# Optimization experiments

Hardware: AMD Instinct MI355X
Metric: run time of the kernel (lower is better)

Reference implementation:

```python
import jax, jax.numpy as jnp
import numpy as np

B, N, NPOINT, NSAMPLE = 8, 8192, 2048, 32
RADIUS = 0.4
C_IN = 64
MLP = [64, 64, 128]
EPS = 1e-5
BIG = 1e10


def setup_inputs() -> dict:
    key = jax.random.key(0)
    ks = jax.random.split(key, 2 + 4 * len(MLP))
    inp = {
        'xyz': jax.random.normal(ks[0], (B, N, 3), jnp.float32),
        'features': jax.random.normal(ks[1], (B, C_IN, N), jnp.float32),
    }
    last_c = C_IN + 3
    j = 2
    for i, out_c in enumerate(MLP):
        inp[f'w{i}'] = jax.random.normal(ks[j], (out_c, last_c), jnp.float32) * (1.0 / np.sqrt(last_c)); j += 1
        inp[f'b{i}'] = jax.random.normal(ks[j], (out_c,), jnp.float32) * 0.01; j += 1
        inp[f'g{i}'] = 1.0 + 0.01 * jax.random.normal(ks[j], (out_c,), jnp.float32); j += 1
        inp[f'bt{i}'] = 0.01 * jax.random.normal(ks[j], (out_c,), jnp.float32); j += 1
        last_c = out_c
    return inp


def fps(xyz, m):
    # Farthest point sampling; deterministic start at index 0 (torch uses randint).
    b, n, _ = xyz.shape

    def step(carry, _):
        dist, far = carry
        centroid = jnp.take_along_axis(xyz, far[:, None, None], axis=1)  # [B,1,3]
        d = jnp.sum((xyz - centroid) ** 2, axis=-1)                      # [B,N]
        dist = jnp.minimum(dist, d)
        new_far = jnp.argmax(dist, axis=1)
        return (dist, new_far), far

    init = (jnp.full((b, n), BIG, xyz.dtype), jnp.zeros((b,), jnp.int32))
    _, idxs = jax.lax.scan(step, init, None, length=m)
    return jnp.transpose(idxs)  # [B,m]


def ball_query(xyz, centroids, radius, k):
    # Euclidean cdist via the (a-b)^2 = a^2 + b^2 - 2ab expansion.
    x2 = jnp.sum(xyz * xyz, axis=-1)            # [B,N]
    c2 = jnp.sum(centroids * centroids, axis=-1)  # [B,M]
    d2 = c2[:, :, None] + x2[:, None, :] - 2.0 * jnp.einsum('bmd,bnd->bmn', centroids, xyz)
    d = jnp.sqrt(jnp.maximum(d2, 0.0))           # [B,M,N]
    dm = jnp.where(d <= radius, d, BIG)
    _, idx = jax.lax.top_k(-dm, k)               # k smallest distances
    return idx                                   # [B,M,K]


def gather_points(x, idx):
    # x: [B,N,C], idx: [B,M,K] -> [B,M,K,C]
    b = x.shape[0]
    return x[jnp.arange(b)[:, None, None], idx]


def reference(xyz, features, w0, b0, g0, bt0, w1, b1, g1, bt1, w2, b2, g2, bt2):
    idx = fps(xyz, NPOINT)                                   # [B,M]
    new_xyz = jnp.take_along_axis(xyz, idx[:, :, None], axis=1)  # [B,M,3]
    knn_idx = ball_query(xyz, new_xyz, RADIUS, NSAMPLE)      # [B,M,K]
    grouped_xyz = gather_points(xyz, knn_idx)                # [B,M,K,3]
    grouped_xyz_norm = grouped_xyz - new_xyz[:, :, None, :]
    grouped_feat = gather_points(jnp.transpose(features, (0, 2, 1)), knn_idx)  # [B,M,K,C]
    feat = jnp.concatenate([grouped_xyz_norm, grouped_feat], axis=-1)          # [B,M,K,C+3]

    for w, b, g, bt in ((w0, b0, g0, bt0), (w1, b1, g1, bt1), (w2, b2, g2, bt2)):
        feat = jnp.einsum('bmkc,oc->bmko', feat, w) + b      # 1x1 conv
        mu = jnp.mean(feat, axis=(0, 1, 2))                  # BN, training-mode batch stats
        var = jnp.mean((feat - mu) ** 2, axis=(0, 1, 2))
        feat = (feat - mu) * jax.lax.rsqrt(var + EPS) * g + bt
        feat = jax.nn.relu(feat)

    new_feat = jnp.max(feat, axis=2)                         # max over neighbors -> [B,M,C_out]
    return new_xyz, jnp.transpose(new_feat, (0, 2, 1))       # [B,M,3], [B,C_out,M]
```

## Files before the change

kernel.cpp:

```cpp
#include <hip/hip_runtime.h>
#include <hip/hip_bf16.h>
#include <stdint.h>

typedef unsigned short u16;
typedef unsigned int   u32;
typedef unsigned long long u64;
typedef float v2f __attribute__((ext_vector_type(2)));
typedef __attribute__((ext_vector_type(8))) short bf16x8;
typedef __attribute__((ext_vector_type(4))) float f32x4;

#define B_    8
#define N_    8192
#define M_    2048
#define NS_   32
#define CIN_  64
#define ROWS_ (B_*M_*NS_)
#define BIGF  1e10f
#define EPSF  1e-5f
#define INV_ROWS (1.0f/524288.0f)

__device__ __forceinline__ u16 f2bf(float f){
  u32 x=__float_as_uint(f);
  return (u16)((x + 0x7FFFu + ((x>>16)&1u))>>16);
}
__device__ __forceinline__ float bf2f(u16 u){ return __uint_as_float(((u32)u)<<16); }

__device__ __forceinline__ u64 wave_max_key(u64 k){
#define DPP_LVL(CTRL) { \
    u32 lo_=(u32)__builtin_amdgcn_update_dpp(0,(int)(u32)k,(CTRL),0xF,0xF,true); \
    u32 hi_=(u32)__builtin_amdgcn_update_dpp(0,(int)(u32)(k>>32),(CTRL),0xF,0xF,true); \
    u64 o_=((u64)hi_<<32)|(u64)lo_; \
    k=(o_>k)?o_:k; }
  DPP_LVL(0x111)
  DPP_LVL(0x112)
  DPP_LVL(0x114)
  DPP_LVL(0x118)
  DPP_LVL(0x142)
  DPP_LVL(0x143)
#undef DPP_LVL
  return k;
}

__global__ __launch_bounds__(256) void k_prep(
    const float* w0,const float* b0,const float* g0,const float* bt0,
    const float* w1,const float* b1,const float* g1,const float* bt1,
    const float* w2,const float* b2,const float* g2,const float* bt2,
    float* biasf,float* gf,float* btf,float* stats,
    u16* Wb0h, u16* Wb0l, u16* Wb1h, u16* Wb1l, u16* Wb2h, u16* Wb2l)
{
  int tid=threadIdx.x;
  for (int i=tid;i<768;i+=256) stats[i]=0.f;
  for (int i=tid;i<6144;i+=256){
    int e=i&7, lane=(i>>3)&63, idx=i>>9;
    int tn=idx/3, k0=idx%3;
    int col = tn*16 + (lane&15);
    int k   = k0*32 + ((lane>>4)&3)*8 + e;
    float v = 0.f;
    if (k < 64)            v = w0[col*67 + 3 + k];
    else if (k < 67)       v = w0[col*67 + (k-64)];
    u16 hib = f2bf(v);
    Wb0h[i] = hib;
    Wb0l[i] = f2bf(v - bf2f(hib));
  }
  for (int i=tid;i<4096;i+=256){
    int e=i&7, lane=(i>>3)&63, k0=(i>>9)&1, tn=i>>10;
    int col = tn*16 + (lane&15);
    int k   = k0*32 + ((lane>>4)&3)*8 + e;
    float v = w1[col*64 + k];
    u16 hib = f2bf(v);
    Wb1h[i] = hib;
    Wb1l[i] = f2bf(v - bf2f(hib));
  }
  for (int i=tid;i<8192;i+=256){
    int e=i&7, lane=(i>>3)&63, k0=(i>>9)&1, tn=i>>10;
    int col = tn*16 + (lane&15);
    int k   = k0*32 + ((lane>>4)&3)*8 + e;
    float v = w2[col*64 + k];
    u16 hib = f2bf(v);
    Wb2h[i] = hib;
    Wb2l[i] = f2bf(v - bf2f(hib));
  }
  if (tid<64){
    biasf[0*128+tid]=b0[tid]; gf[0*128+tid]=g0[tid]; btf[0*128+tid]=bt0[tid];
    biasf[1*128+tid]=b1[tid]; gf[1*128+tid]=g1[tid]; btf[1*128+tid]=bt1[tid];
  }
  if (tid<128){
    biasf[2*128+tid]=b2[tid]; gf[2*128+tid]=g2[tid]; btf[2*128+tid]=bt2[tid];
  }
}

__global__ __launch_bounds__(256) void k_tr(const float* __restrict__ feats, u16* __restrict__ featT)
{
  __shared__ float t[64][65];
  int bb=blockIdx.y, n0=blockIdx.x*64, tid=threadIdx.x;
  int a=tid&63, q=tid>>6;
  const float* fp = feats + (size_t)bb*CIN_*N_;
  #pragma unroll
  for (int s=0;s<16;s++){ int c=q*16+s; t[c][a]=fp[(size_t)c*N_ + n0 + a]; }
  __syncthreads();
  u16* op = featT + (size_t)bb*N_*CIN_;
  #pragma unroll
  for (int s=0;s<16;s++){ int n=q*16+s; op[(size_t)(n0+n)*CIN_ + a] = f2bf(t[a][n]); }
}

__global__ __launch_bounds__(512) void k_fps(const float* __restrict__ xyz,
                                             float* __restrict__ nxyz, float* __restrict__ out0)
{
#pragma clang fp contract(off)
  __shared__ float sx[N_], sy[N_], sz[N_];
  __shared__ int sidx[M_];
  __shared__ u64 skey[2][8];
  int b=blockIdx.x, tid=threadIdx.x;
  const float* xp = xyz + (size_t)b*N_*3;
  for (int i=tid;i<N_;i+=512){ sx[i]=xp[i*3]; sy[i]=xp[i*3+1]; sz[i]=xp[i*3+2]; }
  __syncthreads();
  v2f px[8],py[8],pz[8],md[8];
  int base = tid*16;
  #pragma unroll
  for (int p=0;p<8;p++){
    px[p]=*(const v2f*)&sx[base+2*p];
    py[p]=*(const v2f*)&sy[base+2*p];
    pz[p]=*(const v2f*)&sz[base+2*p];
    v2f m0; m0[0]=BIGF; m0[1]=BIGF; md[p]=m0;
  }
  u32 invb = 0xFFFFFFFFu - (u32)base;
  int far=0;
  int lane=tid&63, wv=tid>>6;
  for (int step=0; step<M_; step++){
    if (tid==0) sidx[step]=far;
    float cxs=sx[far], cys=sy[far], czs=sz[far];
    v2f cx; cx[0]=cxs; cx[1]=cxs;
    v2f cy; cy[0]=cys; cy[1]=cys;
    v2f cz; cz[0]=czs; cz[1]=czs;
    u64 kb=0;
    #pragma unroll
    for (int p=0;p<8;p++){
      v2f dx=px[p]-cx, dy=py[p]-cy, dz=pz[p]-cz;
      v2f d=(dx*dx+dy*dy)+dz*dz;
      v2f m=__builtin_elementwise_min(md[p],d);
      md[p]=m;
      u64 k0=((u64)__float_as_uint(m[0])<<32)|(u64)(invb-(u32)(2*p));
      u64 k1=((u64)__float_as_uint(m[1])<<32)|(u64)(invb-(u32)(2*p+1));
      u64 kp=(k1>k0)?k1:k0;
      kb=(kp>kb)?kp:kb;
    }
    kb = wave_max_key(kb);
    int par = step & 1;
    if (lane==63) skey[par][wv]=kb;
    __syncthreads();
    u64 a0=skey[par][0],a1=skey[par][1],a2=skey[par][2],a3=skey[par][3];
    u64 a4=skey[par][4],a5=skey[par][5],a6=skey[par][6],a7=skey[par][7];
    a0=(a1>a0)?a1:a0; a2=(a3>a2)?a3:a2; a4=(a5>a4)?a5:a4; a6=(a7>a6)?a7:a6;
    a0=(a2>a0)?a2:a0; a4=(a6>a4)?a6:a4;
    a0=(a4>a0)?a4:a0;
    far = (int)(0xFFFFFFFFu - (u32)(a0 & 0xFFFFFFFFull));
  }
  for (int i=tid;i<M_;i+=512){
    int id = sidx[i];
    float x=sx[id], y=sy[id], z=sz[id];
    size_t o=(size_t)(b*M_+i)*3;
    nxyz[o]=x; nxyz[o+1]=y; nxyz[o+2]=z;
    out0[o]=x; out0[o+1]=y; out0[o+2]=z;
  }
}

#define BQCAP 512
__global__ __launch_bounds__(512) void k_bq(const float* __restrict__ xyz, const float* __restrict__ nxyz,
                                            int* __restrict__ knn)
{
  __shared__ float4 sP[N_];
  __shared__ float candd[8][BQCAP];
  __shared__ u16  candi[8][BQCAP];
  int tid=threadIdx.x;
  int cid0 = blockIdx.x*8;
  int b = cid0 >> 11;
  const float* xp = xyz + (size_t)b*N_*3;
  for (int i=tid;i<N_;i+=512){
    float x=xp[i*3], y=xp[i*3+1], z=xp[i*3+2];
    float x2 = __fmul_rn(x,x);
    x2 = __fadd_rn(x2, __fmul_rn(y,y));
    x2 = __fadd_rn(x2, __fmul_rn(z,z));
    sP[i]=make_float4(x,y,z,x2);
  }
  __syncthreads();
  int w=tid>>6, lane=tid&63;
  int cid = cid0 + w;
  float cx=nxyz[(size_t)cid*3], cy=nxyz[(size_t)cid*3+1], cz=nxyz[(size_t)cid*3+2];
  float c2 = __fmul_rn(cx,cx);
  c2 = __fadd_rn(c2, __fmul_rn(cy,cy));
  c2 = __fadd_rn(c2, __fmul_rn(cz,cz));
  int cnt=0;
  for (int i0=0;i0<N_;i0+=64){
    int i=i0+lane;
    float4 p=sP[i];
    float dot = __fmul_rn(cx,p.x);
    dot = __fadd_rn(dot, __fmul_rn(cy,p.y));
    dot = __fadd_rn(dot, __fmul_rn(cz,p.z));
    float d2 = __fsub_rn(__fadd_rn(c2,p.w), __fmul_rn(2.0f,dot));
    float d = sqrtf(fmaxf(d2,0.f));
    bool in = (d <= 0.4f);
    u64 msk = __ballot(in);
    int pos = cnt + __popcll(msk & ((1ull<<lane)-1ull));
    if (in && pos<BQCAP){ candd[w][pos]=d; candi[w][pos]=(u16)i; }
    cnt += __popcll(msk);
  }
  int R = cnt<BQCAP ? cnt : BQCAP;
  int* kout = knn + (size_t)cid*NS_;
  if (R >= NS_){
    for (int s=0;s<NS_;s++){
      u64 kb = ~0ull;
      for (int j=lane;j<R;j+=64){
        float v=candd[w][j];
        u64 k = ((u64)__float_as_uint(v)<<32) | (u64)(u32)j;
        kb = (k<kb)?k:kb;
      }
      u64 inv = wave_max_key(~kb);
      if (lane==63){
        u64 kw = ~inv;
        int bpp = (int)(u32)(kw & 0xFFFFFFFFull);
        kout[s]=candi[w][bpp];
        candd[w][bpp]=3e38f;
      }
    }
  } else {
    if (lane<R) kout[lane]=candi[w][lane];
    int need = NS_-R, slot = R;
    for (int i0=0; i0<N_ && need>0; i0+=64){
      int i=i0+lane;
      float4 p=sP[i];
      float dot = __fmul_rn(cx,p.x);
      dot = __fadd_rn(dot, __fmul_rn(cy,p.y));
      dot = __fadd_rn(dot, __fmul_rn(cz,p.z));
      float d2 = __fsub_rn(__fadd_rn(c2,p.w), __fmul_rn(2.0f,dot));
      float d = sqrtf(fmaxf(d2,0.f));
      bool in = (d <= 0.4f);
      u64 mm = __ballot(!in);
      while (mm && need>0){
        int bpos = __ffsll((long long)mm)-1;
        if (lane==0) kout[slot] = i0+bpos;
        slot++; need--;
        mm &= mm-1;
      }
    }
  }
}

__global__ __launch_bounds__(256) void k_mm0(const float* __restrict__ xyz, const u16* __restrict__ featT,
                                             const int* __restrict__ knn, const float* __restrict__ nxyz,
                                             const u16* __restrict__ Wb0h, const u16* __restrict__ Wb0l,
                                             const float* __restrict__ bias0, u16* __restrict__ Y0)
{
  __shared__ u16 Xs[64*128];
  __shared__ u16 WH[12*64*8];
  __shared__ u16 WL[12*64*8];
  int tid=threadIdx.x;
  {
    const uint4* s4=(const uint4*)Wb0h; uint4* d4=(uint4*)WH;
    const uint4* s5=(const uint4*)Wb0l; uint4* d5=(uint4*)WL;
    for (int i=tid;i<768;i+=256){ d4[i]=s4[i]; d5[i]=s5[i]; }
  }
  size_t base=(size_t)blockIdx.x*64;
  {
    int rl=tid>>2, t=tid&3;
    int row=(int)base+rl;
    int bm = row>>5, b = row>>16;
    int n  = knn[row];
    const uint4* fp = (const uint4*)(featT + ((size_t)b*N_ + n)*CIN_);
    char* xr = (char*)Xs + rl*256;
    u32 swz = (u32)((rl&7)<<4);
    uint4 v0=fp[t*2], v1=fp[t*2+1];
    *(uint4*)(xr + ((t*32)    ^ swz)) = v0;
    *(uint4*)(xr + ((t*32+16) ^ swz)) = v1;
    uint4 pz = make_uint4(0u,0u,0u,0u);
    if (t==0){
      const float* cp = nxyz + (size_t)bm*3;
      const float* xp = xyz + ((size_t)b*N_ + n)*3;
      u32 w01 = (u32)f2bf(xp[0]-cp[0]) | ((u32)f2bf(xp[1]-cp[1])<<16);
      u32 w2  = (u32)f2bf(xp[2]-cp[2]);
      pz.x = w01; pz.y = w2;
    }
    *(uint4*)(xr + ((128+t*16) ^ swz)) = pz;
  }
  __syncthreads();
  int w=tid>>6, lane=tid&63;
  f32x4 acc[4];
  #pragma unroll
  for (int tn=0;tn<4;tn++){ acc[tn][0]=0.f; acc[tn][1]=0.f; acc[tn][2]=0.f; acc[tn][3]=0.f; }
  int arow = w*16 + (lane&15);
  u32 aswz = (u32)((arow&7)<<4);
  #pragma unroll
  for (int k0=0;k0<3;k0++){
    int aoff = arow*256 + (int)(((u32)((k0*32 + ((lane>>4)&3)*8)*2)) ^ aswz);
    bf16x8 a = *(const bf16x8*)((const char*)Xs + aoff);
    #pragma unroll
    for (int tn=0;tn<4;tn++){
      bf16x8 bl = *(const bf16x8*)&WL[((tn*3+k0)*64+lane)*8];
      bf16x8 bh = *(const bf16x8*)&WH[((tn*3+k0)*64+lane)*8];
      acc[tn] = __builtin_amdgcn_mfma_f32_16x16x32_bf16(a, bl, acc[tn], 0,0,0);
      acc[tn] = __builtin_amdgcn_mfma_f32_16x16x32_bf16(a, bh, acc[tn], 0,0,0);
    }
  }
  #pragma unroll
  for (int tn=0;tn<4;tn++){
    int col = tn*16 + (lane&15);
    float bb = bias0[col];
    #pragma unroll
    for (int j=0;j<4;j++){
      int row = w*16 + (lane>>4)*4 + j;
      Y0[(base+row)*64 + col] = f2bf(acc[tn][j] + bb);
    }
  }
}

template<int C>
__global__ __launch_bounds__(256) void k_stats(const u16* __restrict__ Y, float* __restrict__ statsOut)
{
  __shared__ float sred[4][128];
  int tid=threadIdx.x;
  int c0=(tid&7)*8;
  int rg=tid>>3;
  float s[8], ss[8];
  #pragma unroll
  for (int k=0;k<8;k++){ s[k]=0.f; ss[k]=0.f; }
  for (size_t r=(size_t)blockIdx.x*32+rg; r<ROWS_; r+=(size_t)gridDim.x*32){
    uint4 v=*(const uint4*)&Y[r*64+c0];
    u32 a[4]={v.x,v.y,v.z,v.w};
    #pragma unroll
    for (int q=0;q<4;q++){
      float lo=bf2f((u16)(a[q]&0xFFFFu));
      float hi=bf2f((u16)(a[q]>>16));
      s[q*2]+=lo;   ss[q*2]+=lo*lo;
      s[q*2+1]+=hi; ss[q*2+1]+=hi*hi;
    }
  }
  #pragma unroll
  for (int off=32; off>=8; off>>=1){
    #pragma unroll
    for (int k=0;k<8;k++){
      s[k]+=__shfl_down(s[k],off);
      ss[k]+=__shfl_down(ss[k],off);
    }
  }
  int lane=tid&63, wv=tid>>6;
  if (lane<8){
    #pragma unroll
    for (int k=0;k<8;k++){
      int ch=lane*8+k;
      sred[wv][ch]=s[k];
      sred[wv][64+ch]=ss[k];
    }
  }
  __syncthreads();
  if (tid<128){
    float a=sred[0][tid]+sred[1][tid]+sred[2][tid]+sred[3][tid];
    int ch=tid&63, which=tid>>6;
    atomicAdd(&statsOut[ch*2+which], a);
  }
}

__global__ __launch_bounds__(256) void k_mm1(u16* __restrict__ Y,
                                             const u16* __restrict__ Wb1h, const u16* __restrict__ Wb1l,
                                             const float* __restrict__ bias1, const float* __restrict__ gf0,
                                             const float* __restrict__ btf0, const float* __restrict__ stats0)
{
  __shared__ u16 Xs[64*64];
  __shared__ u16 WH[8*64*8];
  __shared__ u16 WL[8*64*8];
  __shared__ float sc[64], sh[64];
  int tid=threadIdx.x;
  if (tid<64){
    float mu = stats0[tid*2]*INV_ROWS;
    float var= stats0[tid*2+1]*INV_ROWS - mu*mu;
    float rs = 1.0f/sqrtf(var+EPSF);
    float s  = rs*gf0[tid];
    sc[tid]=s; sh[tid]=btf0[tid]-mu*s;
  }
  {
    const uint4* sh4=(const uint4*)Wb1h; uint4* dh4=(uint4*)WH;
    const uint4* sl4=(const uint4*)Wb1l; uint4* dl4=(uint4*)WL;
    dh4[tid]=sh4[tid]; dh4[tid+256]=sh4[tid+256];
    dl4[tid]=sl4[tid]; dl4[tid+256]=sl4[tid+256];
  }
  __syncthreads();
  size_t base=(size_t)blockIdx.x*64;
  for (int i=tid;i<512;i+=256){
    int rl=i>>3, c0=(i&7)*8;
    uint4 v=*(const uint4*)(Y + (base+rl)*64 + c0);
    u32 arr[4]={v.x,v.y,v.z,v.w};
    u32 pk[4];
    #pragma unroll
    for (int q=0;q<4;q++){
      int cc=c0+q*2;
      float lo=bf2f((u16)(arr[q]&0xFFFFu));
      float hi=bf2f((u16)(arr[q]>>16));
      lo=fmaxf(0.f, lo*sc[cc]+sh[cc]);
      hi=fmaxf(0.f, hi*sc[cc+1]+sh[cc+1]);
      pk[q] = (u32)f2bf(lo) | ((u32)f2bf(hi)<<16);
    }
    uint4 o4; o4.x=pk[0]; o4.y=pk[1]; o4.z=pk[2]; o4.w=pk[3];
    int byteoff = rl*128 + ((c0*2) ^ ((rl&7)<<4));
    *(uint4*)((char*)Xs + byteoff) = o4;
  }
  __syncthreads();
  int w=tid>>6, lane=tid&63;
  f32x4 acc[4];
  #pragma unroll
  for (int tn=0;tn<4;tn++){ acc[tn][0]=0.f; acc[tn][1]=0.f; acc[tn][2]=0.f; acc[tn][3]=0.f; }
  int arow = w*16 + (lane&15);
  #pragma unroll
  for (int k0=0;k0<2;k0++){
    int aoff = arow*128 + ((k0*64 + (lane>>4)*16) ^ ((arow&7)<<4));
    bf16x8 a = *(const bf16x8*)((const char*)Xs + aoff);
    #pragma unroll
    for (int tn=0;tn<4;tn++){
      bf16x8 bl = *(const bf16x8*)&WL[((tn*2+k0)*64+lane)*8];
      bf16x8 bh = *(const bf16x8*)&WH[((tn*2+k0)*64+lane)*8];
      acc[tn] = __builtin_amdgcn_mfma_f32_16x16x32_bf16(a, bl, acc[tn], 0,0,0);
      acc[tn] = __builtin_amdgcn_mfma_f32_16x16x32_bf16(a, bh, acc[tn], 0,0,0);
    }
  }
  #pragma unroll
  for (int tn=0;tn<4;tn++){
    int col = tn*16 + (lane&15);
    float bb = bias1[col];
    #pragma unroll
    for (int j=0;j<4;j++){
      int row = w*16 + (lane>>4)*4 + j;
      Y[(base+row)*64 + col] = f2bf(acc[tn][j] + bb);
    }
  }
}

__global__ __launch_bounds__(256) void k_mm2a(const u16* __restrict__ Y1,
                                              const u16* __restrict__ Wb2h, const u16* __restrict__ Wb2l,
                                              const float* __restrict__ bias2, const float* __restrict__ gf1,
                                              const float* __restrict__ btf1, const float* __restrict__ stats1,
                                              float* __restrict__ stats2, float* __restrict__ out1)
{
  __shared__ u16 Xs[64*64];
  __shared__ u16 WH[8192];
  __shared__ u16 WL[8192];
  __shared__ float Ys[64*128];
  __shared__ float sc[64], sh[64];
  __shared__ float sred[512];
  int tid=threadIdx.x;
  if (tid<64){
    float mu = stats1[tid*2]*INV_ROWS;
    float var= stats1[tid*2+1]*INV_ROWS - mu*mu;
    float rs = 1.0f/sqrtf(var+EPSF);
    float s  = rs*gf1[tid];
    sc[tid]=s; sh[tid]=btf1[tid]-mu*s;
  }
  {
    const uint4* s4=(const uint4*)Wb2h; uint4* d4=(uint4*)WH;
    const uint4* s5=(const uint4*)Wb2l; uint4* d5=(uint4*)WL;
    for (int i=tid;i<1024;i+=256){ d4[i]=s4[i]; d5[i]=s5[i]; }
  }
  int w=tid>>6, lane=tid&63;
  int pg=tid>>7, po=tid&127;
  float accSum=0.f, accSq=0.f;
  __syncthreads();
  for (int tile=blockIdx.x; tile<8192; tile+=gridDim.x){
    size_t base=(size_t)tile*64;
    for (int i=tid;i<512;i+=256){
      int rl=i>>3, c0=(i&7)*8;
      uint4 v=*(const uint4*)(Y1 + (base+rl)*64 + c0);
      u32 arr[4]={v.x,v.y,v.z,v.w};
      u32 pk[4];
      #pragma unroll
      for (int q=0;q<4;q++){
        int cc=c0+q*2;
        float lo=bf2f((u16)(arr[q]&0xFFFFu));
        float hi=bf2f((u16)(arr[q]>>16));
        lo=fmaxf(0.f, lo*sc[cc]+sh[cc]);
        hi=fmaxf(0.f, hi*sc[cc+1]+sh[cc+1]);
        pk[q] = (u32)f2bf(lo) | ((u32)f2bf(hi)<<16);
      }
      uint4 o4; o4.x=pk[0]; o4.y=pk[1]; o4.z=pk[2]; o4.w=pk[3];
      int byteoff = rl*128 + ((c0*2) ^ ((rl&7)<<4));
      *(uint4*)((char*)Xs + byteoff) = o4;
    }
    __syncthreads();
    f32x4 acc[8];
    #pragma unroll
    for (int tn=0;tn<8;tn++){ acc[tn][0]=0.f; acc[tn][1]=0.f; acc[tn][2]=0.f; acc[tn][3]=0.f; }
    int arow = w*16 + (lane&15);
    #pragma unroll
    for (int k0=0;k0<2;k0++){
      int aoff = arow*128 + ((k0*64 + (lane>>4)*16) ^ ((arow&7)<<4));
      bf16x8 a = *(const bf16x8*)((const char*)Xs + aoff);
      #pragma unroll
      for (int tn=0;tn<8;tn++){
        bf16x8 bl = *(const bf16x8*)&WL[((tn*2+k0)*64+lane)*8];
        bf16x8 bh = *(const bf16x8*)&WH[((tn*2+k0)*64+lane)*8];
        acc[tn] = __builtin_amdgcn_mfma_f32_16x16x32_bf16(a, bl, acc[tn], 0,0,0);
        acc[tn] = __builtin_amdgcn_mfma_f32_16x16x32_bf16(a, bh, acc[tn], 0,0,0);
      }
    }
    #pragma unroll
    for (int tn=0;tn<8;tn++){
      int col = tn*16 + (lane&15);
      float bb = bias2[col];
      #pragma unroll
      for (int j=0;j<4;j++){
        int row = w*16 + (lane>>4)*4 + j;
        int byteoff = row*512 + ((col*4) ^ ((row&7)<<4));
        *(float*)((char*)Ys + byteoff) = acc[tn][j] + bb;
      }
    }
    __syncthreads();
    {
      float mx=-3e38f;
      #pragma unroll 4
      for (int k=0;k<32;k++){
        int row = pg*32 + k;
        int byteoff = row*512 + ((po*4) ^ ((row&7)<<4));
        float y = *(const float*)((const char*)Ys + byteoff);
        accSum += y; accSq += y*y;
        mx = fmaxf(mx, y);
      }
      int bm = tile*2 + pg; int bi = bm>>11, m = bm&2047;
      out1[((size_t)bi*128+po)*M_ + m] = mx;
    }
    __syncthreads();
  }
  sred[tid]      = accSum;
  sred[256+tid]  = accSq;
  __syncthreads();
  if (tid<128){
    float s = sred[tid] + sred[tid+128];
    float q = sred[256+tid] + sred[256+tid+128];
    atomicAdd(&stats2[tid*2],   s);
    atomicAdd(&stats2[tid*2+1], q);
  }
}

__global__ __launch_bounds__(256) void k_pool(float* __restrict__ out1, const float* __restrict__ stats2,
                                              const float* __restrict__ gf2, const float* __restrict__ btf2)
{
  int idx = blockIdx.x*256 + threadIdx.x;
  int o = (idx >> 11) & 127;
  float mu = stats2[o*2]*INV_ROWS;
  float var= stats2[o*2+1]*INV_ROWS - mu*mu;
  float rs = 1.0f/sqrtf(var+EPSF);
  float s  = rs*gf2[o];
  float sh = btf2[o]-mu*s;
  out1[idx] = fmaxf(0.f, out1[idx]*s + sh);
}

extern "C" void kernel_launch(void* const* d_in, const int* in_sizes, int n_in,
                              void* d_out, int out_size, void* d_ws, size_t ws_size,
                              hipStream_t stream)
{
  (void)in_sizes; (void)n_in; (void)out_size; (void)ws_size;
  const float* xyz =(const float*)d_in[0];
  const float* feat=(const float*)d_in[1];
  const float* w0=(const float*)d_in[2],  *b0=(const float*)d_in[3],  *g0=(const float*)d_in[4],  *bt0=(const float*)d_in[5];
  const float* w1=(const float*)d_in[6],  *b1=(const float*)d_in[7],  *g1=(const float*)d_in[8],  *bt1=(const float*)d_in[9];
  const float* w2=(const float*)d_in[10], *b2=(const float*)d_in[11], *g2=(const float*)d_in[12], *bt2=(const float*)d_in[13];
  float* out0=(float*)d_out;
  float* out1=out0 + (size_t)B_*M_*3;

  char* ws=(char*)d_ws;
  float* nxyz =(float*)(ws);
  u16*   Wb1h =(u16*)  (ws + 196608);
  u16*   Wb1l =(u16*)  (ws + 204800);
  u16*   Wb2h =(u16*)  (ws + 212992);
  u16*   Wb2l =(u16*)  (ws + 229376);
  int*   knn  =(int*)  (ws + 262144);
  u16*   Wb0h =(u16*)  (ws + 2359296);
  u16*   Wb0l =(u16*)  (ws + 2376704);
  float* biasf=(float*)(ws + 2425856);
  float* gfp  =(float*)(ws + 2427392);
  float* btfp =(float*)(ws + 2428928);
  float* stats=(float*)(ws + 2430464);
  u16*   featT=(u16*)  (ws + 2433536);
  u16*   Y0   =(u16*)  (ws + 10822144);

  k_prep<<<1,256,0,stream>>>(w0,b0,g0,bt0,w1,b1,g1,bt1,w2,b2,g2,bt2,biasf,gfp,btfp,stats,
                             Wb0h,Wb0l,Wb1h,Wb1l,Wb2h,Wb2l);
  k_tr<<<dim3(128,8),256,0,stream>>>(feat, featT);
  k_fps<<<B_,512,0,stream>>>(xyz, nxyz, out0);
  k_bq<<<2048,512,0,stream>>>(xyz, nxyz, knn);
  k_mm0<<<8192,256,0,stream>>>(xyz, featT, knn, nxyz, Wb0h, Wb0l, biasf+0, Y0);
  k_stats<64><<<128,256,0,stream>>>(Y0, stats+0);
  k_mm1<<<8192,256,0,stream>>>(Y0, Wb1h, Wb1l, biasf+128, gfp+0, btfp+0, stats+0);
  k_stats<64><<<128,256,0,stream>>>(Y0, stats+256);
  k_mm2a<<<512,256,0,stream>>>(Y0, Wb2h, Wb2l, biasf+256, gfp+128, btfp+128, stats+256, stats+512, out1);
  k_pool<<<8192,256,0,stream>>>(out1, stats+512, gfp+256, btfp+256);
}
```

Before: 2.316 ms.

## Spatially bin points in FPS and skip waves whose bounding box cannot improve

The FPS kernel now reorders each batch's points into shared memory by a 64-cell octant/quantile code, so each wave holds a spatially compact cluster, and computes a per-wave bounding box. At each step a wave skips its distance update and reduction when the lower-bound distance from the centroid to its box exceeds the wave's current max min-distance, reusing the cached key instead. Tie-breaking is kept by encoding the original index into the key's low bits along with the sorted position. The binning thresholds assume roughly standard-normal coordinates, and the saving depends on how often waves can skip. The per-step barrier is still there.

```diff
diff --git a/kernel.cpp b/kernel.cpp
--- a/kernel.cpp
+++ b/kernel.cpp
@@ -110,12 +110,41 @@
   __shared__ float sx[N_], sy[N_], sz[N_];
   __shared__ int sidx[M_];
   __shared__ u64 skey[2][8];
+  __shared__ u32 hist[64];
+  __shared__ u32 cptr[64];
+  __shared__ u16 sOrg[N_];
+  __shared__ int sFar0;
   int b=blockIdx.x, tid=threadIdx.x;
   const float* xp = xyz + (size_t)b*N_*3;
-  for (int i=tid;i<N_;i+=512){ sx[i]=xp[i*3]; sy[i]=xp[i*3+1]; sz[i]=xp[i*3+2]; }
-  __syncthreads();
+  if (tid<64) hist[tid]=0;
+  __syncthreads();
+  for (int i=tid;i<N_;i+=512){
+    float x=xp[i*3], y=xp[i*3+1], z=xp[i*3+2];
+    int bx = (x<0.f) ? (x<-0.6745f?0:1) : (x<0.6745f?2:3);
+    int by = (y<0.f) ? (y<-0.6745f?0:1) : (y<0.6745f?2:3);
+    int bz = (z<0.f) ? (z<-0.6745f?0:1) : (z<0.6745f?2:3);
+    int code = ((bx>>1)<<5)|((by>>1)<<4)|((bz>>1)<<3)|((bx&1)<<2)|((by&1)<<1)|(bz&1);
+    atomicAdd(&hist[code],1u);
+  }
+  __syncthreads();
+  if (tid==0){ u32 run=0; for (int c=0;c<64;c++){ cptr[c]=run; run+=hist[c]; } }
+  __syncthreads();
+  for (int i=tid;i<N_;i+=512){
+    float x=xp[i*3], y=xp[i*3+1], z=xp[i*3+2];
+    int bx = (x<0.f) ? (x<-0.6745f?0:1) : (x<0.6745f?2:3);
+    int by = (y<0.f) ? (y<-0.6745f?0:1) : (y<0.6745f?2:3);
+    int bz = (z<0.f) ? (z<-0.6745f?0:1) : (z<0.6745f?2:3);
+    int code = ((bx>>1)<<5)|((by>>1)<<4)|((bz>>1)<<3)|((bx&1)<<2)|((by&1)<<1)|(bz&1);
+    u32 pos = atomicAdd(&cptr[code],1u);
+    sx[pos]=x; sy[pos]=y; sz[pos]=z; sOrg[pos]=(u16)i;
+    if (i==0) sFar0=(int)pos;
+  }
+  __syncthreads();
+  int lane=tid&63, wv=tid>>6;
+  const int permA[8]={0,2,4,6,1,3,5,7};
+  int base = permA[wv]*1024 + lane*16;
   v2f px[8],py[8],pz[8],md[8];
-  int base = tid*16;
+  u32 klow[16];
   #pragma unroll
   for (int p=0;p<8;p++){
     px[p]=*(const v2f*)&sx[base+2*p];
@@ -123,37 +152,66 @@
     pz[p]=*(const v2f*)&sz[base+2*p];
     v2f m0; m0[0]=BIGF; m0[1]=BIGF; md[p]=m0;
   }
-  u32 invb = 0xFFFFFFFFu - (u32)base;
-  int far=0;
-  int lane=tid&63, wv=tid>>6;
+  #pragma unroll
+  for (int j=0;j<16;j++){
+    u32 org=(u32)sOrg[base+j];
+    klow[j] = ((0x1FFFu-org)<<13) | (u32)(base+j);
+  }
+  float bxlo,bxhi,bylo,byhi,bzlo,bzhi;
+  {
+    float xl=px[0][0],xh=px[0][0],yl=py[0][0],yh=py[0][0],zl=pz[0][0],zh=pz[0][0];
+    #pragma unroll
+    for (int p=0;p<8;p++){
+      xl=fminf(xl,fminf(px[p][0],px[p][1])); xh=fmaxf(xh,fmaxf(px[p][0],px[p][1]));
+      yl=fminf(yl,fminf(py[p][0],py[p][1])); yh=fmaxf(yh,fmaxf(py[p][0],py[p][1]));
+      zl=fminf(zl,fminf(pz[p][0],pz[p][1])); zh=fmaxf(zh,fmaxf(pz[p][0],pz[p][1]));
+    }
+    #pragma unroll
+    for (int off=32;off>0;off>>=1){
+      xl=fminf(xl,__shfl_xor(xl,off)); xh=fmaxf(xh,__shfl_xor(xh,off));
+      yl=fminf(yl,__shfl_xor(yl,off)); yh=fmaxf(yh,__shfl_xor(yh,off));
+      zl=fminf(zl,__shfl_xor(zl,off)); zh=fmaxf(zh,__shfl_xor(zh,off));
+    }
+    bxlo=xl; bxhi=xh; bylo=yl; byhi=yh; bzlo=zl; bzhi=zh;
+  }
+  int far=sFar0;
+  u64 kb_reg=0;
+  float gmaxf=3.9e38f;
   for (int step=0; step<M_; step++){
     if (tid==0) sidx[step]=far;
     float cxs=sx[far], cys=sy[far], czs=sz[far];
-    v2f cx; cx[0]=cxs; cx[1]=cxs;
-    v2f cy; cy[0]=cys; cy[1]=cys;
-    v2f cz; cz[0]=czs; cz[1]=czs;
-    u64 kb=0;
-    #pragma unroll
-    for (int p=0;p<8;p++){
-      v2f dx=px[p]-cx, dy=py[p]-cy, dz=pz[p]-cz;
-      v2f d=(dx*dx+dy*dy)+dz*dz;
-      v2f m=__builtin_elementwise_min(md[p],d);
-      md[p]=m;
-      u64 k0=((u64)__float_as_uint(m[0])<<32)|(u64)(invb-(u32)(2*p));
-      u64 k1=((u64)__float_as_uint(m[1])<<32)|(u64)(invb-(u32)(2*p+1));
-      u64 kp=(k1>k0)?k1:k0;
-      kb=(kp>kb)?kp:kb;
-    }
-    kb = wave_max_key(kb);
+    float ddx = fmaxf(fmaxf(bxlo-cxs, cxs-bxhi), 0.f);
+    float ddy = fmaxf(fmaxf(bylo-cys, cys-byhi), 0.f);
+    float ddz = fmaxf(fmaxf(bzlo-czs, czs-bzhi), 0.f);
+    float lb2 = (ddx*ddx+ddy*ddy)+ddz*ddz;
+    if (!(lb2*0.99999f >= gmaxf)){
+      v2f cx; cx[0]=cxs; cx[1]=cxs;
+      v2f cy; cy[0]=cys; cy[1]=cys;
+      v2f cz; cz[0]=czs; cz[1]=czs;
+      u64 kb=0;
+      #pragma unroll
+      for (int p=0;p<8;p++){
+        v2f dx=px[p]-cx, dy=py[p]-cy, dz=pz[p]-cz;
+        v2f d=(dx*dx+dy*dy)+dz*dz;
+        v2f m=__builtin_elementwise_min(md[p],d);
+        md[p]=m;
+        u64 k0=((u64)__float_as_uint(m[0])<<32)|(u64)klow[2*p];
+        u64 k1=((u64)__float_as_uint(m[1])<<32)|(u64)klow[2*p+1];
+        u64 kp=(k1>k0)?k1:k0;
+        kb=(kp>kb)?kp:kb;
+      }
+      kb_reg = wave_max_key(kb);
+      gmaxf = __uint_as_float((u32)__builtin_amdgcn_readlane((int)(u32)(kb_reg>>32),63));
+    }
     int par = step & 1;
-    if (lane==63) skey[par][wv]=kb;
+    if (lane==63) skey[par][wv]=kb_reg;
     __syncthreads();
     u64 a0=skey[par][0],a1=skey[par][1],a2=skey[par][2],a3=skey[par][3];
     u64 a4=skey[par][4],a5=skey[par][5],a6=skey[par][6],a7=skey[par][7];
     a0=(a1>a0)?a1:a0; a2=(a3>a2)?a3:a2; a4=(a5>a4)?a5:a4; a6=(a7>a6)?a7:a6;
     a0=(a2>a0)?a2:a0; a4=(a6>a4)?a6:a4;
     a0=(a4>a0)?a4:a0;
-    far = (int)(0xFFFFFFFFu - (u32)(a0 & 0xFFFFFFFFull));
+    far = (int)(a0 & 0x1FFFull);
   }
   for (int i=tid;i<M_;i+=512){
     int id = sidx[i];
```

Result: slower. 2.363 ms (+2.0%).
